# Kernel optimization log

Measured on AMD Instinct MI355X. Metric: run time of the kernel, lower is better.

## Reference

```python
import jax, jax.numpy as jnp
import numpy as np

N, G, P, E = 65536, 256, 256, 1048576   # nodes, graphs, nodes/graph, edges
AF, BF, D, H, L, CE, T = 92, 41, 64, 128, 3, 16, 4
EPS = 1e-5


def _lin(x, W, b):
    return x @ W + b


def setup_inputs() -> dict:
    key = jax.random.key(0)
    ks = jax.random.split(key, 32)
    f = jax.random.normal
    inp = {
        "x": f(ks[0], (N, AF), jnp.float32),
        "edge_attr": f(ks[1], (E, BF), jnp.float32),
        "charge": f(ks[2], (G,), jnp.float32),
        "charge_W": f(ks[3], (1, CE)) * 0.3,
        "charge_b": f(ks[4], (CE,)) * 0.1,
        "atom_W": f(ks[5], (AF + CE, D)) * (1.0 / np.sqrt(AF + CE)),
        "atom_b": f(ks[6], (D,)) * 0.1,
        "bond_W": f(ks[7], (BF, D)) * (1.0 / np.sqrt(BF)),
        "bond_b": f(ks[8], (D,)) * 0.1,
        "nu_W1": f(ks[9], (L, 2 * D, D)) * (1.0 / np.sqrt(2 * D)),
        "nu_b1": f(ks[10], (L, D)) * 0.1,
        "nu_W2": f(ks[11], (L, D, D)) * (1.0 / np.sqrt(D)),
        "nu_b2": f(ks[12], (L, D)) * 0.1,
        "eu_W1": f(ks[13], (L, 3 * D, D)) * (1.0 / np.sqrt(3 * D)),
        "eu_b1": f(ks[14], (L, D)) * 0.1,
        "eu_W2": f(ks[15], (L, D, D)) * (1.0 / np.sqrt(D)),
        "eu_b2": f(ks[16], (L, D)) * 0.1,
        "bn_gamma": jnp.ones((L, D), jnp.float32),
        "bn_beta": jnp.zeros((L, D), jnp.float32),
        "pred_W1": f(ks[17], (D, H)) * (1.0 / np.sqrt(D)),
        "pred_b1": f(ks[18], (H,)) * 0.1,
        "pred_W2": f(ks[19], (H, H)) * (1.0 / np.sqrt(H)),
        "pred_b2": f(ks[20], (H,)) * 0.1,
        "pred_W3": f(ks[21], (H, 1)) * (1.0 / np.sqrt(H)),
        "pred_b3": f(ks[22], (1,)) * 0.1,
        "edge_index": jax.random.randint(ks[23], (2, E), 0, N, jnp.int32),
        "batch": (jnp.arange(N, dtype=jnp.int32) // P),
        "target_site_indices": jax.random.randint(ks[24], (G, T), 0, P, jnp.int32),
    }
    return inp


def reference(x, edge_attr, charge, charge_W, charge_b, atom_W, atom_b, bond_W,
              bond_b, nu_W1, nu_b1, nu_W2, nu_b2, eu_W1, eu_b1, eu_W2, eu_b2,
              bn_gamma, bn_beta, pred_W1, pred_b1, pred_W2, pred_b2, pred_W3,
              pred_b3, edge_index, batch, target_site_indices):
    sp = jax.nn.softplus
    # early charge integration
    charge_feat = _lin(charge[:, None], charge_W, charge_b)        # [G, CE]
    h = _lin(jnp.concatenate([x, charge_feat[batch]], 1), atom_W, atom_b)  # [N, D]
    e = _lin(edge_attr, bond_W, bond_b)                            # [E, D]
    row, col = edge_index[0], edge_index[1]
    for i in range(L):
        hs, hd = h[row], h[col]                                    # gather per edge
        e = _lin(sp(_lin(jnp.concatenate([hs, hd, e], 1), eu_W1[i], eu_b1[i])),
                 eu_W2[i], eu_b2[i])                               # edge update
        m = _lin(sp(_lin(jnp.concatenate([hs, e], 1), nu_W1[i], nu_b1[i])),
                 nu_W2[i], nu_b2[i])                               # messages
        hn = jax.ops.segment_sum(m, col, num_segments=N)           # scatter_add
        mu = hn.mean(0)
        var = hn.var(0)                                            # biased, as torch BN train
        hn = (hn - mu) / jnp.sqrt(var + EPS) * bn_gamma[i] + bn_beta[i]
        h = sp(hn) + h
    # selective pooling over target sites (vectorized version of per-graph loop)
    counts = jax.ops.segment_sum(jnp.ones((N,), h.dtype), batch, num_segments=G)
    counts_i = counts.astype(jnp.int32)
    starts = (jnp.cumsum(counts_i) - counts_i)                     # [G] graph offsets
    valid = target_site_indices < counts_i[:, None]                # [G, T]
    gidx = starts[:, None] + jnp.where(valid, target_site_indices, 0)
    sel = h[gidx] * valid[:, :, None].astype(h.dtype)              # [G, T, D]
    nsel = valid.sum(1)
    sel_mean = sel.sum(1) / jnp.maximum(nsel, 1)[:, None].astype(h.dtype)
    gmean = jax.ops.segment_sum(h, batch, num_segments=G) / counts[:, None]
    graph_repr = jnp.where((nsel > 0)[:, None], sel_mean, gmean)   # [G, D]
    # predictor (dropout = identity in eval)
    z = sp(_lin(graph_repr, pred_W1, pred_b1))
    z = sp(_lin(z, pred_W2, pred_b2))
    out = _lin(z, pred_W3, pred_b3)
    return out.squeeze(-1)                                         # [G]
```

## Files before the change

kernel.cpp:

```cpp
#include <hip/hip_runtime.h>
#include <hip/hip_bf16.h>
#include <hip/hip_fp16.h>
#include <math.h>

#define N_NODES 65536
#define N_GRAPH 256
#define P_NODES 256
#define N_EDGES 1048576
#define AF 92
#define BF 41
#define DIM 64
#define HID 128
#define NLAYER 3
#define CE 16
#define TS 4
#define BN_EPS 1e-5f
#define EPW 32
#define PSTRIDE 33

typedef _Float16 half8 __attribute__((ext_vector_type(8)));
typedef float floatx4 __attribute__((ext_vector_type(4)));

__device__ __forceinline__ float softplus_f(float x) {
    return fmaxf(x, 0.0f) + __logf(1.0f + __expf(-fabsf(x)));
}

__global__ __launch_bounds__(64) void k_h0(
    const float* __restrict__ x, const float* __restrict__ charge,
    const float* __restrict__ chW, const float* __restrict__ chb,
    const float* __restrict__ atomW, const float* __restrict__ atomb,
    const int* __restrict__ batch, float* __restrict__ h)
{
    const int n = blockIdx.x * 64 + threadIdx.x;
    float acc[DIM];
#pragma unroll
    for (int j = 0; j < DIM; ++j) acc[j] = atomb[j];
    const float* xr = x + (size_t)n * AF;
    for (int k2 = 0; k2 < AF; k2 += 2) {
        float2 a = *(const float2*)(xr + k2);
        {
            const float* w = atomW + (size_t)k2 * DIM;
#pragma unroll
            for (int j = 0; j < DIM; ++j) acc[j] = fmaf(w[j], a.x, acc[j]);
        }
        {
            const float* w = atomW + (size_t)(k2 + 1) * DIM;
#pragma unroll
            for (int j = 0; j < DIM; ++j) acc[j] = fmaf(w[j], a.y, acc[j]);
        }
    }
    const float cg = charge[batch[n]];
#pragma unroll
    for (int k = 0; k < CE; ++k) {
        float av = fmaf(cg, chW[k], chb[k]);
        const float* w = atomW + (size_t)(AF + k) * DIM;
#pragma unroll
        for (int j = 0; j < DIM; ++j) acc[j] = fmaf(w[j], av, acc[j]);
    }
    float* hp = h + (size_t)n * DIM;
#pragma unroll
    for (int j = 0; j < DIM; j += 4)
        *(float4*)(hp + j) = make_float4(acc[j], acc[j+1], acc[j+2], acc[j+3]);
}

__global__ __launch_bounds__(256) void k_hist(const int* __restrict__ ecol,
                                              int* __restrict__ cnt)
{
    int t = blockIdx.x * 256 + threadIdx.x;
    atomicAdd(&cnt[ecol[t]], 1);
}

__global__ __launch_bounds__(256) void k_scan(const int* __restrict__ cnt,
                                              int* __restrict__ starts)
{
    __shared__ int ps[256];
    const int t = threadIdx.x;
    int s = 0;
    for (int i = 0; i < 256; ++i) s += cnt[t * 256 + i];
    ps[t] = s;
    __syncthreads();
    for (int off = 1; off < 256; off <<= 1) {
        int v = (t >= off) ? ps[t - off] : 0;
        __syncthreads();
        ps[t] += v;
        __syncthreads();
    }
    int run = ps[t] - s;
    for (int i = 0; i < 256; ++i) {
        starts[t * 256 + i] = run;
        run += cnt[t * 256 + i];
    }
    if (t == 255) starts[N_NODES] = run;
}

__global__ __launch_bounds__(256) void k_scatter(const int* __restrict__ ecol,
                                                 int* __restrict__ cur,
                                                 int* __restrict__ perm,
                                                 int* __restrict__ ipos)
{
    int t = blockIdx.x * 256 + threadIdx.x;
    int pos = atomicAdd(&cur[ecol[t]], 1);
    perm[pos] = t;
    ipos[t] = pos;
}

__global__ __launch_bounds__(256) void k_wprep_all(
    const float* __restrict__ euW1, const float* __restrict__ euW2,
    const float* __restrict__ nuW1, const float* __restrict__ nuW2,
    __half* __restrict__ out)
{
    const int idx = blockIdx.x * 256 + threadIdx.x;
    const int layer = idx / 28672;
    int off = idx - layer * 28672;
    const float* W;
    if (off < 12288)        { W = euW1 + (size_t)layer * 192 * DIM; }
    else if (off < 16384)   { W = euW2 + (size_t)layer * DIM * DIM; off -= 12288; }
    else if (off < 24576)   { W = nuW1 + (size_t)layer * 128 * DIM; off -= 16384; }
    else                    { W = nuW2 + (size_t)layer * DIM * DIM; off -= 24576; }
    int j    = off & 7;
    int lane = (off >> 3) & 63;
    int f    = off >> 9;
    int ntile = f & 3;
    int kIter = f >> 2;
    int k = kIter * 32 + ((lane >> 4) & 3) * 8 + j;
    int n = ntile * 16 + (lane & 15);
    out[idx] = __float2half(W[k * 64 + n]);
}

__global__ __launch_bounds__(256) void k_wprep_bond(
    const float* __restrict__ bondW, __half* __restrict__ out)
{
    const int idx = blockIdx.x * 256 + threadIdx.x;
    int j    = idx & 7;
    int lane = (idx >> 3) & 63;
    int f    = idx >> 9;
    int ntile = f & 3;
    int kIter = f >> 2;
    int k = kIter * 32 + ((lane >> 4) & 3) * 8 + j;
    int n = ntile * 16 + (lane & 15);
    out[idx] = (k < BF) ? __float2half(bondW[k * 64 + n]) : __float2half(0.0f);
}

__device__ __forceinline__ void init_acc(floatx4 acc[2][4],
                                         const float* __restrict__ b, int mrow)
{
#pragma unroll
    for (int n = 0; n < 4; ++n) {
        float bv = b[n * 16 + mrow];
        floatx4 f = {bv, bv, bv, bv};
        acc[0][n] = f;
        acc[1][n] = f;
    }
}

__device__ __forceinline__ void gemm_panel(floatx4 acc[2][4],
                                           const _Float16* __restrict__ P,
                                           const __half* __restrict__ Wf,
                                           int fragBase, int quad,
                                           int mrow, int lane)
{
    const _Float16* Wh = (const _Float16*)Wf;
#pragma unroll
    for (int ki = 0; ki < 2; ++ki) {
        const _Float16* pa = P + (size_t)(((ki * 4 + quad) * PSTRIDE + mrow) * 8);
        half8 a0 = *(const half8*)pa;
        half8 a1 = *(const half8*)(pa + 16 * 8);
#pragma unroll
        for (int n = 0; n < 4; ++n) {
            half8 b = *(const half8*)(Wh +
                ((size_t)(fragBase + ki * 4 + n) * 64 + lane) * 8);
            acc[0][n] = __builtin_amdgcn_mfma_f32_16x16x32_f16(a0, b, acc[0][n], 0, 0, 0);
            acc[1][n] = __builtin_amdgcn_mfma_f32_16x16x32_f16(a1, b, acc[1][n], 0, 0, 0);
        }
    }
}

__device__ __forceinline__ void cstore_panel(const floatx4 acc[2][4],
                                             _Float16* __restrict__ P,
                                             int quad, int mrow, bool sp)
{
#pragma unroll
    for (int t = 0; t < 2; ++t)
#pragma unroll
        for (int n = 0; n < 4; ++n)
#pragma unroll
            for (int r = 0; r < 4; ++r) {
                int edge = t * 16 + quad * 4 + r;
                int d = n * 16 + mrow;
                float v = acc[t][n][r];
                if (sp) v = softplus_f(v);
                P[((d >> 3) * PSTRIDE + edge) * 8 + (d & 7)] = (_Float16)v;
            }
}

__device__ __forceinline__ void rows_to_global(const _Float16* __restrict__ P,
                                               __half* __restrict__ dst,
                                               int e0, int lane)
{
#pragma unroll
    for (int i = 0; i < 4; ++i) {
        int idx = i * 64 + lane;
        int eL = idx >> 3;
        int c  = idx & 7;
        half8 v = *(const half8*)&P[(c * PSTRIDE + eL) * 8];
        *(half8*)((_Float16*)dst + (size_t)(e0 + eL) * 64 + c * 8) = v;
    }
}

__device__ __forceinline__ void stage_h(const float* __restrict__ hrow,
                                        _Float16* __restrict__ P,
                                        int sEdge, int sSeg)
{
    const float* hp = hrow + sSeg * 32;
#pragma unroll
    for (int i = 0; i < 4; ++i) {
        float4 v0 = *(const float4*)(hp + i * 8);
        float4 v1 = *(const float4*)(hp + i * 8 + 4);
        half8 hv;
        hv[0] = (_Float16)v0.x; hv[1] = (_Float16)v0.y;
        hv[2] = (_Float16)v0.z; hv[3] = (_Float16)v0.w;
        hv[4] = (_Float16)v1.x; hv[5] = (_Float16)v1.y;
        hv[6] = (_Float16)v1.z; hv[7] = (_Float16)v1.w;
        *(half8*)&P[((sSeg * 4 + i) * PSTRIDE + sEdge) * 8] = hv;
    }
}

__device__ __forceinline__ void stage_e2(_Float16* __restrict__ P,
                                         int id2, float2 v)
{
    int idx = id2 * 2;
    int e = (idx * 51151) >> 21;
    int k = idx - e * 41;
    P[((k >> 3) * PSTRIDE + e) * 8 + (k & 7)] = (_Float16)v.x;
    idx++;
    e = (idx * 51151) >> 21;
    k = idx - e * 41;
    P[((k >> 3) * PSTRIDE + e) * 8 + (k & 7)] = (_Float16)v.y;
}

__global__ __launch_bounds__(64) void k_e0m(
    const float* __restrict__ eattr, const __half* __restrict__ Wb,
    const float* __restrict__ bondb, const int* __restrict__ ipos,
    __half* __restrict__ eT)
{
    __shared__ __align__(16) _Float16 P0[8 * PSTRIDE * 8];
    __shared__ int slot[32];
    const int lane = threadIdx.x;
    const int quad = lane >> 4;
    const int mrow = lane & 15;
    const int e0   = blockIdx.x * 32;

    if (lane < 32) slot[lane] = ipos[e0 + lane];

    {
        half8 z = {};
#pragma unroll
        for (int i = 0; i < 4; ++i) ((half8*)P0)[i * 64 + lane] = z;
        if (lane < 8) ((half8*)P0)[256 + lane] = z;
    }
    __syncthreads();

    const float* src = eattr + (size_t)e0 * BF;
#pragma unroll
    for (int i = 0; i < 10; ++i) {
        const int id2 = i * 64 + lane;
        float2 v = *(const float2*)(src + id2 * 2);
        stage_e2(P0, id2, v);
    }
    if (lane < 16) {
        const int id2 = 640 + lane;
        float2 v = *(const float2*)(src + id2 * 2);
        stage_e2(P0, id2, v);
    }
    __syncthreads();

    floatx4 acc[2][4];
    init_acc(acc, bondb, mrow);
    gemm_panel(acc, P0, Wb, 0, quad, mrow, lane);
    __syncthreads();
    cstore_panel(acc, P0, quad, mrow, false);
    __syncthreads();

#pragma unroll
    for (int i = 0; i < 4; ++i) {
        int idx = i * 64 + lane;
        int eL = idx >> 3;
        int c  = idx & 7;
        half8 v = *(const half8*)&P0[(c * PSTRIDE + eL) * 8];
        *(half8*)((_Float16*)eT + (size_t)slot[eL] * DIM + c * 8) = v;
    }
}

__global__ __launch_bounds__(64) void k_edge4(
    const float* __restrict__ h, __half* __restrict__ eT,
    const __half* __restrict__ Wf,
    const float* __restrict__ eub1, const float* __restrict__ eub2,
    const float* __restrict__ nub1, const float* __restrict__ nub2,
    const int* __restrict__ erow, const int* __restrict__ ecol,
    const int* __restrict__ perm,
    __half* __restrict__ m)
{
    __shared__ __align__(16) _Float16 P0[8 * PSTRIDE * 8];
    __shared__ __align__(16) _Float16 P1[8 * PSTRIDE * 8];
    const int lane = threadIdx.x;
    const int quad = lane >> 4;
    const int mrow = lane & 15;
    const int e0   = blockIdx.x * EPW;
    const int sEdge = lane >> 1;
    const int sSeg  = lane & 1;

    floatx4 acc[2][4];

    half8 epre[4];
    {
        const _Float16* ep = (const _Float16*)(eT + (size_t)(e0 + sEdge) * DIM) + sSeg * 32;
#pragma unroll
        for (int i = 0; i < 4; ++i) epre[i] = *(const half8*)(ep + i * 8);
    }

    const int ed = perm[e0 + sEdge];
    stage_h(h + (size_t)erow[ed] * DIM, P0, sEdge, sSeg);
    stage_h(h + (size_t)ecol[ed] * DIM, P1, sEdge, sSeg);
    __syncthreads();

    init_acc(acc, eub1, mrow);
    gemm_panel(acc, P0, Wf, 0, quad, mrow, lane);
    gemm_panel(acc, P1, Wf, 8, quad, mrow, lane);
    __syncthreads();
    {
#pragma unroll
        for (int i = 0; i < 4; ++i)
            *(half8*)&P1[((sSeg * 4 + i) * PSTRIDE + sEdge) * 8] = epre[i];
    }
    __syncthreads();
    gemm_panel(acc, P1, Wf, 16, quad, mrow, lane);
    __syncthreads();
    cstore_panel(acc, P1, quad, mrow, true);
    __syncthreads();

    init_acc(acc, eub2, mrow);
    gemm_panel(acc, P1, Wf, 24, quad, mrow, lane);
    __syncthreads();
    cstore_panel(acc, P1, quad, mrow, false);
    __syncthreads();
    rows_to_global(P1, eT, e0, lane);

    init_acc(acc, nub1, mrow);
    gemm_panel(acc, P0, Wf, 32, quad, mrow, lane);
    gemm_panel(acc, P1, Wf, 40, quad, mrow, lane);
    __syncthreads();
    cstore_panel(acc, P0, quad, mrow, true);
    __syncthreads();

    init_acc(acc, nub2, mrow);
    gemm_panel(acc, P0, Wf, 48, quad, mrow, lane);
    __syncthreads();
    cstore_panel(acc, P1, quad, mrow, false);
    __syncthreads();
    rows_to_global(P1, m, e0, lane);
}

__global__ __launch_bounds__(256) void k_agg(
    const __half2* __restrict__ m2, const int* __restrict__ starts,
    float* __restrict__ hn)
{
    const int w = threadIdx.x >> 6;
    const int lane = threadIdx.x & 63;
    const int n = blockIdx.x * 4 + w;
    const int s = starts[n], e = starts[n + 1];
    const int r = lane >> 5, d2 = lane & 31;
    float ax = 0.f, ay = 0.f;
    for (int i = s + r; i < e; i += 2) {
        float2 f = __half22float2(m2[(size_t)i * 32 + d2]);
        ax += f.x; ay += f.y;
    }
    ax += __shfl(ax, lane ^ 32, 64);
    ay += __shfl(ay, lane ^ 32, 64);
    if (r == 0) *(float2*)(hn + (size_t)n * DIM + d2 * 2) = make_float2(ax, ay);
}

__global__ __launch_bounds__(256) void k_bnstats(const float* __restrict__ hn,
                                                 float* __restrict__ stats)
{
    const int j = threadIdx.x & 63;
    const int sub = threadIdx.x >> 6;
    const int r0 = blockIdx.x * 256;
    float s = 0.f, qq = 0.f;
    for (int i = 0; i < 64; ++i) {
        float v = hn[(size_t)(r0 + i * 4 + sub) * DIM + j];
        s += v;
        qq = fmaf(v, v, qq);
    }
    __shared__ float ls[256], lq[256];
    ls[threadIdx.x] = s; lq[threadIdx.x] = qq;
    __syncthreads();
    if (threadIdx.x < 128) {
        ls[threadIdx.x] += ls[threadIdx.x + 128];
        lq[threadIdx.x] += lq[threadIdx.x + 128];
    }
    __syncthreads();
    if (threadIdx.x < 64) {
        atomicAdd(&stats[j],      ls[threadIdx.x] + ls[threadIdx.x + 64]);
        atomicAdd(&stats[64 + j], lq[threadIdx.x] + lq[threadIdx.x + 64]);
    }
}

__global__ __launch_bounds__(256) void k_hupd(
    const float* __restrict__ hn, float* __restrict__ h,
    const float* __restrict__ stats, const float* __restrict__ gamma,
    const float* __restrict__ beta)
{
    const size_t idx = (size_t)blockIdx.x * 256 + threadIdx.x;
    const int j = (int)(idx & 63);
    const float inv_n = 1.0f / (float)N_NODES;
    float mu  = stats[j] * inv_n;
    float var = stats[64 + j] * inv_n - mu * mu;
    float sc  = gamma[j] * rsqrtf(var + BN_EPS);
    float v   = (hn[idx] - mu) * sc + beta[j];
    h[idx] += softplus_f(v);
}

__global__ __launch_bounds__(64) void k_pool(const float* __restrict__ h,
                                             const int* __restrict__ tsi,
                                             float* __restrict__ gr)
{
    const int g = blockIdx.x, j = threadIdx.x;
    float s = 0.f;
#pragma unroll
    for (int t = 0; t < TS; ++t) {
        int p = tsi[g * TS + t];
        s += h[(size_t)(g * P_NODES + p) * DIM + j];
    }
    gr[g * DIM + j] = s * (1.0f / TS);
}

__global__ __launch_bounds__(128) void k_pred(const float* __restrict__ gr,
    const float* __restrict__ W1, const float* __restrict__ b1,
    const float* __restrict__ W2, const float* __restrict__ b2,
    const float* __restrict__ W3, const float* __restrict__ b3,
    float* __restrict__ out)
{
    const int g = blockIdx.x, j = threadIdx.x;
    __shared__ float zin[DIM], z1[HID], red[HID];
    if (j < DIM) zin[j] = gr[g * DIM + j];
    __syncthreads();
    float a = b1[j];
    for (int k = 0; k < DIM; ++k) a = fmaf(zin[k], W1[k * HID + j], a);
    z1[j] = softplus_f(a);
    __syncthreads();
    float a2 = b2[j];
    for (int k = 0; k < HID; ++k) a2 = fmaf(z1[k], W2[k * HID + j], a2);
    red[j] = softplus_f(a2) * W3[j];
    __syncthreads();
    for (int s = 64; s > 0; s >>= 1) {
        if (j < s) red[j] += red[j + s];
        __syncthreads();
    }
    if (j == 0) out[g] = red[0] + b3[0];
}

extern "C" void kernel_launch(void* const* d_in, const int* in_sizes, int n_in,
                              void* d_out, int out_size, void* d_ws, size_t ws_size,
                              hipStream_t stream)
{
    const float* x      = (const float*)d_in[0];
    const float* eattr  = (const float*)d_in[1];
    const float* charge = (const float*)d_in[2];
    const float* chW    = (const float*)d_in[3];
    const float* chb    = (const float*)d_in[4];
    const float* atomW  = (const float*)d_in[5];
    const float* atomb  = (const float*)d_in[6];
    const float* bondW  = (const float*)d_in[7];
    const float* bondb  = (const float*)d_in[8];
    const float* nuW1   = (const float*)d_in[9];
    const float* nub1   = (const float*)d_in[10];
    const float* nuW2   = (const float*)d_in[11];
    const float* nub2   = (const float*)d_in[12];
    const float* euW1   = (const float*)d_in[13];
    const float* eub1   = (const float*)d_in[14];
    const float* euW2   = (const float*)d_in[15];
    const float* eub2   = (const float*)d_in[16];
    const float* gamma  = (const float*)d_in[17];
    const float* beta   = (const float*)d_in[18];
    const float* pW1    = (const float*)d_in[19];
    const float* pb1    = (const float*)d_in[20];
    const float* pW2    = (const float*)d_in[21];
    const float* pb2    = (const float*)d_in[22];
    const float* pW3    = (const float*)d_in[23];
    const float* pb3    = (const float*)d_in[24];
    const int*   eidx   = (const int*)d_in[25];
    const int*   batch  = (const int*)d_in[26];
    const int*   tsi    = (const int*)d_in[27];
    const int* erow = eidx;
    const int* ecol = eidx + N_EDGES;

    char* ws = (char*)d_ws;
    float*  h      = (float*)(ws);
    float*  hn     = (float*)(ws + ((size_t)16 << 20));
    int*    ipos   = (int*)  (ws + ((size_t)16 << 20));
    float*  stats  = (float*)(ws + ((size_t)32 << 20));
    float*  gr     = (float*)(ws + ((size_t)32 << 20) + (64 << 10));
    int*    counts = (int*)  (ws + ((size_t)33 << 20));
    int*    starts = (int*)  (ws + ((size_t)33 << 20) + (256 << 10));
    int*    cur    = (int*)  (ws + ((size_t)33 << 20) + (768 << 10));
    __half* Wfrag  = (__half*)(ws + ((size_t)34 << 20));
    __half* Wbond  = (__half*)(ws + ((size_t)34 << 20) + (256 << 10));
    int*    perm   = (int*)  (ws + ((size_t)35 << 20));
    __half* eT     = (__half*)(ws + ((size_t)40 << 20));
    __half* m      = (__half*)(ws + ((size_t)168 << 20));

    hipMemsetAsync(counts, 0, N_NODES * sizeof(int), stream);
    k_hist<<<N_EDGES / 256, 256, 0, stream>>>(ecol, counts);
    k_scan<<<1, 256, 0, stream>>>(counts, starts);
    hipMemcpyAsync(cur, starts, N_NODES * sizeof(int),
                   hipMemcpyDeviceToDevice, stream);
    k_scatter<<<N_EDGES / 256, 256, 0, stream>>>(ecol, cur, perm, ipos);

    k_wprep_all<<<(3 * 28672) / 256, 256, 0, stream>>>(euW1, euW2, nuW1, nuW2, Wfrag);
    k_wprep_bond<<<16, 256, 0, stream>>>(bondW, Wbond);

    k_h0<<<N_NODES / 64, 64, 0, stream>>>(x, charge, chW, chb, atomW, atomb, batch, h);
    k_e0m<<<N_EDGES / 32, 64, 0, stream>>>(eattr, Wbond, bondb, ipos, eT);

    const size_t LW = 28672;
    for (int i = 0; i < NLAYER; ++i) {
        hipMemsetAsync(stats, 0, 128 * sizeof(float), stream);
        k_edge4<<<N_EDGES / EPW, 64, 0, stream>>>(h, eT, Wfrag + i * LW,
            eub1 + i * DIM, eub2 + i * DIM, nub1 + i * DIM, nub2 + i * DIM,
            erow, ecol, perm, m);
        k_agg<<<N_NODES / 4, 256, 0, stream>>>((const __half2*)m, starts, hn);
        k_bnstats<<<N_NODES / 256, 256, 0, stream>>>(hn, stats);
        k_hupd<<<(N_NODES * DIM) / 256, 256, 0, stream>>>(hn, h, stats,
            gamma + i * DIM, beta + i * DIM);
    }

    k_pool<<<N_GRAPH, 64, 0, stream>>>(h, tsi, gr);
    k_pred<<<N_GRAPH, HID, 0, stream>>>(gr, pW1, pb1, pW2, pb2, pW3, pb3, (float*)d_out);
}
```

Measured before the change: 1.327 ms.

## Fold edge W2 into node W1, keep fp16 node copy, parallelize scan

The edge-update second linear layer and the edge half of the node MLP's first layer are folded into one precomputed 64x64 weight and bias. The node MLP can then run directly from the edge-MLP hidden activations, and the edge output GEMM overlaps with it. A separate fp16 copy of h is maintained so edge kernels gather half-size rows. Messages are stored in the MFMA-native layout and hn becomes fp16, so aggregation and BN passes move less data. The single-block scan is split into a three-kernel parallel scan. Changing the order of operations and using fp16 for hn and the fused weights may alter numerics slightly.

Measured after the change: 1.278 ms. 3.7% less time.

```diff
diff --git a/kernel.cpp b/kernel.cpp
--- a/kernel.cpp
+++ b/kernel.cpp
@@ -19,6 +19,7 @@
 #define PSTRIDE 33
 
 typedef _Float16 half8 __attribute__((ext_vector_type(8)));
+typedef _Float16 half4_t __attribute__((ext_vector_type(4)));
 typedef float floatx4 __attribute__((ext_vector_type(4)));
 
 __device__ __forceinline__ float softplus_f(float x) {
@@ -29,7 +30,8 @@
     const float* __restrict__ x, const float* __restrict__ charge,
     const float* __restrict__ chW, const float* __restrict__ chb,
     const float* __restrict__ atomW, const float* __restrict__ atomb,
-    const int* __restrict__ batch, float* __restrict__ h)
+    const int* __restrict__ batch, float* __restrict__ h,
+    __half* __restrict__ h16)
 {
     const int n = blockIdx.x * 64 + threadIdx.x;
     float acc[DIM];
@@ -58,9 +60,17 @@
         for (int j = 0; j < DIM; ++j) acc[j] = fmaf(w[j], av, acc[j]);
     }
     float* hp = h + (size_t)n * DIM;
+    _Float16* hq = (_Float16*)h16 + (size_t)n * DIM;
 #pragma unroll
     for (int j = 0; j < DIM; j += 4)
         *(float4*)(hp + j) = make_float4(acc[j], acc[j+1], acc[j+2], acc[j+3]);
+#pragma unroll
+    for (int j = 0; j < DIM; j += 8) {
+        half8 hv;
+#pragma unroll
+        for (int u = 0; u < 8; ++u) hv[u] = (_Float16)acc[j + u];
+        *(half8*)(hq + j) = hv;
+    }
 }
 
 __global__ __launch_bounds__(256) void k_hist(const int* __restrict__ ecol,
@@ -70,27 +80,53 @@
     atomicAdd(&cnt[ecol[t]], 1);
 }
 
-__global__ __launch_bounds__(256) void k_scan(const int* __restrict__ cnt,
-                                              int* __restrict__ starts)
+__global__ __launch_bounds__(256) void k_blksum(const int* __restrict__ cnt,
+                                                int* __restrict__ bs)
+{
+    __shared__ int red[256];
+    red[threadIdx.x] = cnt[blockIdx.x * 256 + threadIdx.x];
+    __syncthreads();
+    for (int o = 128; o > 0; o >>= 1) {
+        if (threadIdx.x < o) red[threadIdx.x] += red[threadIdx.x + o];
+        __syncthreads();
+    }
+    if (threadIdx.x == 0) bs[blockIdx.x] = red[0];
+}
+
+__global__ __launch_bounds__(256) void k_scanb(const int* __restrict__ bs,
+                                               int* __restrict__ bo)
 {
     __shared__ int ps[256];
     const int t = threadIdx.x;
-    int s = 0;
-    for (int i = 0; i < 256; ++i) s += cnt[t * 256 + i];
-    ps[t] = s;
+    int v = bs[t];
+    ps[t] = v;
     __syncthreads();
     for (int off = 1; off < 256; off <<= 1) {
-        int v = (t >= off) ? ps[t - off] : 0;
+        int u = (t >= off) ? ps[t - off] : 0;
         __syncthreads();
-        ps[t] += v;
+        ps[t] += u;
         __syncthreads();
     }
-    int run = ps[t] - s;
-    for (int i = 0; i < 256; ++i) {
-        starts[t * 256 + i] = run;
-        run += cnt[t * 256 + i];
-    }
-    if (t == 255) starts[N_NODES] = run;
+    bo[t] = ps[t] - v;
+}
+
+__global__ __launch_bounds__(256) void k_scan3(const int* __restrict__ cnt,
+                                               const int* __restrict__ bo,
+                                               int* __restrict__ starts)
+{
+    __shared__ int ps[256];
+    const int b = blockIdx.x, t = threadIdx.x;
+    int v = cnt[b * 256 + t];
+    ps[t] = v;
+    __syncthreads();
+    for (int off = 1; off < 256; off <<= 1) {
+        int u = (t >= off) ? ps[t - off] : 0;
+        __syncthreads();
+        ps[t] += u;
+        __syncthreads();
+    }
+    starts[b * 256 + t] = bo[b] + ps[t] - v;
+    if (b == 255 && t == 255) starts[N_NODES] = bo[255] + ps[255];
 }
 
 __global__ __launch_bounds__(256) void k_scatter(const int* __restrict__ ecol,
@@ -141,6 +177,45 @@
     out[idx] = (k < BF) ? __float2half(bondW[k * 64 + n]) : __float2half(0.0f);
 }
 
+__global__ __launch_bounds__(64) void k_wfuse(
+    const float* __restrict__ euW2, const float* __restrict__ nuW1,
+    const float* __restrict__ eub2, const float* __restrict__ nub1,
+    float* __restrict__ WfuF32, float* __restrict__ bfu)
+{
+    const int L = blockIdx.x, j = threadIdx.x;
+    const float* W2  = euW2 + (size_t)L * DIM * DIM;
+    const float* N1b = nuW1 + (size_t)L * 128 * DIM + 64 * DIM;
+    float acc[64];
+#pragma unroll
+    for (int k = 0; k < 64; ++k) acc[k] = 0.f;
+    for (int l = 0; l < 64; ++l) {
+        float nv = N1b[l * 64 + j];
+#pragma unroll
+        for (int k = 0; k < 64; ++k) acc[k] = fmaf(W2[k * 64 + l], nv, acc[k]);
+    }
+    float* outW = WfuF32 + (size_t)L * 4096;
+    for (int k = 0; k < 64; ++k) outW[k * 64 + j] = acc[k];
+    float b = nub1[L * 64 + j];
+    for (int l = 0; l < 64; ++l) b = fmaf(eub2[L * 64 + l], N1b[l * 64 + j], b);
+    bfu[L * 64 + j] = b;
+}
+
+__global__ __launch_bounds__(256) void k_wprep_fuse(
+    const float* __restrict__ WfuF32, __half* __restrict__ out)
+{
+    const int idx = blockIdx.x * 256 + threadIdx.x;
+    const int layer = idx >> 12;
+    int off = idx & 4095;
+    int j    = off & 7;
+    int lane = (off >> 3) & 63;
+    int f    = off >> 9;
+    int ntile = f & 3;
+    int kIter = f >> 2;
+    int k = kIter * 32 + ((lane >> 4) & 3) * 8 + j;
+    int n = ntile * 16 + (lane & 15);
+    out[idx] = __float2half(WfuF32[(size_t)layer * 4096 + k * 64 + n]);
+}
+
 __device__ __forceinline__ void init_acc(floatx4 acc[2][4],
                                          const float* __restrict__ b, int mrow)
 {
@@ -207,22 +282,172 @@
     }
 }
 
-__device__ __forceinline__ void stage_h(const float* __restrict__ hrow,
-                                        _Float16* __restrict__ P,
-                                        int sEdge, int sSeg)
-{
-    const float* hp = hrow + sSeg * 32;
+__device__ __forceinline__ void store_m_native(const floatx4 acc[2][4],
+        __half* __restrict__ m, int blk, int quad, int mrow)
+{
+    _Float16* base = (_Float16*)m + (size_t)blk * 2048;
+#pragma unroll
+    for (int t = 0; t < 2; ++t)
+#pragma unroll
+        for (int n = 0; n < 4; ++n) {
+            half4_t hv;
+            hv[0] = (_Float16)acc[t][n][0];
+            hv[1] = (_Float16)acc[t][n][1];
+            hv[2] = (_Float16)acc[t][n][2];
+            hv[3] = (_Float16)acc[t][n][3];
+            *(half4_t*)(base + ((((t * 4 + n) * 4 + quad) * 16 + mrow) * 4)) = hv;
+        }
+}
+
+__device__ __forceinline__ void stage_h16(const __half* __restrict__ hrow,
+                                          _Float16* __restrict__ P,
+                                          int sEdge, int sSeg)
+{
+    const _Float16* hp = (const _Float16*)hrow + sSeg * 32;
 #pragma unroll
     for (int i = 0; i < 4; ++i) {
-        float4 v0 = *(const float4*)(hp + i * 8);
-        float4 v1 = *(const float4*)(hp + i * 8 + 4);
-        half8 hv;
-        hv[0] = (_Float16)v0.x; hv[1] = (_Float16)v0.y;
-        hv[2] = (_Float16)v0.z; hv[3] = (_Float16)v0.w;
-        hv[4] = (_Float16)v1.x; hv[5] = (_Float16)v1.y;
-        hv[6] = (_Float16)v1.z; hv[7] = (_Float16)v1.w;
+        half8 hv = *(const half8*)(hp + i * 8);
         *(half8*)&P[((sSeg * 4 + i) * PSTRIDE + sEdge) * 8] = hv;
     }
+}
+
+__global__ __launch_bounds__(64, 4) void k_edge4(
+    const __half* __restrict__ h16, __half* __restrict__ eT,
+    const __half* __restrict__ Wf, const __half* __restrict__ Wfu,
+    const float* __restrict__ eub1, const float* __restrict__ eub2,
+    const float* __restrict__ bfu,  const float* __restrict__ nub2,
+    const int* __restrict__ erow, const int* __restrict__ ecol,
+    const int* __restrict__ perm,
+    __half* __restrict__ m)
+{
+    __shared__ __align__(16) _Float16 P0[8 * PSTRIDE * 8];
+    __shared__ __align__(16) _Float16 P1[8 * PSTRIDE * 8];
+    const int lane = threadIdx.x;
+    const int quad = lane >> 4;
+    const int mrow = lane & 15;
+    const int e0   = blockIdx.x * EPW;
+    const int sEdge = lane >> 1;
+    const int sSeg  = lane & 1;
+
+    floatx4 acc[2][4], acc2[2][4];
+
+    half8 epre[4];
+    {
+        const _Float16* ep = (const _Float16*)(eT + (size_t)(e0 + sEdge) * DIM) + sSeg * 32;
+#pragma unroll
+        for (int i = 0; i < 4; ++i) epre[i] = *(const half8*)(ep + i * 8);
+    }
+
+    const int ed = perm[e0 + sEdge];
+    stage_h16(h16 + (size_t)erow[ed] * DIM, P0, sEdge, sSeg);
+    stage_h16(h16 + (size_t)ecol[ed] * DIM, P1, sEdge, sSeg);
+    __syncthreads();
+
+    init_acc(acc, eub1, mrow);
+    gemm_panel(acc, P0, Wf, 0, quad, mrow, lane);
+    gemm_panel(acc, P1, Wf, 8, quad, mrow, lane);
+    __syncthreads();
+    {
+#pragma unroll
+        for (int i = 0; i < 4; ++i)
+            *(half8*)&P1[((sSeg * 4 + i) * PSTRIDE + sEdge) * 8] = epre[i];
+    }
+    __syncthreads();
+    gemm_panel(acc, P1, Wf, 16, quad, mrow, lane);
+    __syncthreads();
+    cstore_panel(acc, P1, quad, mrow, true);
+    __syncthreads();
+
+    init_acc(acc, bfu, mrow);
+    gemm_panel(acc, P0, Wf, 32, quad, mrow, lane);
+    gemm_panel(acc, P1, Wfu, 0, quad, mrow, lane);
+    init_acc(acc2, eub2, mrow);
+    gemm_panel(acc2, P1, Wf, 24, quad, mrow, lane);
+    __syncthreads();
+    cstore_panel(acc, P0, quad, mrow, true);
+    __syncthreads();
+
+    init_acc(acc, nub2, mrow);
+    gemm_panel(acc, P0, Wf, 48, quad, mrow, lane);
+    __syncthreads();
+    cstore_panel(acc2, P1, quad, mrow, false);
+    __syncthreads();
+    rows_to_global(P1, eT, e0, lane);
+    store_m_native(acc, m, blockIdx.x, quad, mrow);
+}
+
+__global__ __launch_bounds__(256) void k_agg(
+    const __half* __restrict__ m, const int* __restrict__ starts,
+    __half* __restrict__ hn)
+{
+    const int w = threadIdx.x >> 6;
+    const int lane = threadIdx.x & 63;
+    const int n = blockIdx.x * 4 + w;
+    const int s = starts[n], e = starts[n + 1];
+    const int nn = lane >> 4, mrow = lane & 15;
+    float acc = 0.f;
+    for (int g = s & ~3; g < e; g += 4) {
+        int blk = g >> 5;
+        int off = g & 31;
+        int t = off >> 4, quad = (off >> 2) & 3;
+        half4_t v = *(const half4_t*)((const _Float16*)m + (size_t)blk * 2048
+                     + (((t * 4 + nn) * 4 + quad) * 16 + mrow) * 4);
+        float f0 = (float)v[0], f1 = (float)v[1];
+        float f2 = (float)v[2], f3 = (float)v[3];
+        if (g >= s && g + 3 < e) {
+            acc += (f0 + f1) + (f2 + f3);
+        } else {
+            if (g     >= s && g     < e) acc += f0;
+            if (g + 1 >= s && g + 1 < e) acc += f1;
+            if (g + 2 >= s && g + 2 < e) acc += f2;
+            if (g + 3 >= s && g + 3 < e) acc += f3;
+        }
+    }
+    hn[(size_t)n * DIM + lane] = (__half)acc;
+}
+
+__global__ __launch_bounds__(256) void k_bnstats(const __half* __restrict__ hn,
+                                                 float* __restrict__ stats)
+{
+    const int j = threadIdx.x & 63;
+    const int sub = threadIdx.x >> 6;
+    const int r0 = blockIdx.x * 256;
+    float s = 0.f, qq = 0.f;
+    for (int i = 0; i < 64; ++i) {
+        float v = (float)hn[(size_t)(r0 + i * 4 + sub) * DIM + j];
+        s += v;
+        qq = fmaf(v, v, qq);
+    }
+    __shared__ float ls[256], lq[256];
+    ls[threadIdx.x] = s; lq[threadIdx.x] = qq;
+    __syncthreads();
+    if (threadIdx.x < 128) {
+        ls[threadIdx.x] += ls[threadIdx.x + 128];
+        lq[threadIdx.x] += lq[threadIdx.x + 128];
+    }
+    __syncthreads();
+    if (threadIdx.x < 64) {
+        atomicAdd(&stats[j],      ls[threadIdx.x] + ls[threadIdx.x + 64]);
+        atomicAdd(&stats[64 + j], lq[threadIdx.x] + lq[threadIdx.x + 64]);
+    }
+}
+
+__global__ __launch_bounds__(256) void k_hupd(
+    const __half* __restrict__ hn, float* __restrict__ h,
+    __half* __restrict__ h16,
+    const float* __restrict__ stats, const float* __restrict__ gamma,
+    const float* __restrict__ beta)
+{
+    const size_t idx = (size_t)blockIdx.x * 256 + threadIdx.x;
+    const int j = (int)(idx & 63);
+    const float inv_n = 1.0f / (float)N_NODES;
+    float mu  = stats[j] * inv_n;
+    float var = stats[64 + j] * inv_n - mu * mu;
+    float sc  = gamma[j] * rsqrtf(var + BN_EPS);
+    float v   = ((float)hn[idx] - mu) * sc + beta[j];
+    float nh  = h[idx] + softplus_f(v);
+    h[idx] = nh;
+    h16[idx] = (__half)nh;
 }
 
 __device__ __forceinline__ void stage_e2(_Float16* __restrict__ P,
@@ -289,135 +514,6 @@
         half8 v = *(const half8*)&P0[(c * PSTRIDE + eL) * 8];
         *(half8*)((_Float16*)eT + (size_t)slot[eL] * DIM + c * 8) = v;
     }
-}
-
-__global__ __launch_bounds__(64) void k_edge4(
-    const float* __restrict__ h, __half* __restrict__ eT,
-    const __half* __restrict__ Wf,
-    const float* __restrict__ eub1, const float* __restrict__ eub2,
-    const float* __restrict__ nub1, const float* __restrict__ nub2,
-    const int* __restrict__ erow, const int* __restrict__ ecol,
-    const int* __restrict__ perm,
-    __half* __restrict__ m)
-{
-    __shared__ __align__(16) _Float16 P0[8 * PSTRIDE * 8];
-    __shared__ __align__(16) _Float16 P1[8 * PSTRIDE * 8];
-    const int lane = threadIdx.x;
-    const int quad = lane >> 4;
-    const int mrow = lane & 15;
-    const int e0   = blockIdx.x * EPW;
-    const int sEdge = lane >> 1;
-    const int sSeg  = lane & 1;
-
-    floatx4 acc[2][4];
-
-    half8 epre[4];
-    {
-        const _Float16* ep = (const _Float16*)(eT + (size_t)(e0 + sEdge) * DIM) + sSeg * 32;
-#pragma unroll
-        for (int i = 0; i < 4; ++i) epre[i] = *(const half8*)(ep + i * 8);
-    }
-
-    const int ed = perm[e0 + sEdge];
-    stage_h(h + (size_t)erow[ed] * DIM, P0, sEdge, sSeg);
-    stage_h(h + (size_t)ecol[ed] * DIM, P1, sEdge, sSeg);
-    __syncthreads();
-
-    init_acc(acc, eub1, mrow);
-    gemm_panel(acc, P0, Wf, 0, quad, mrow, lane);
-    gemm_panel(acc, P1, Wf, 8, quad, mrow, lane);
-    __syncthreads();
-    {
-#pragma unroll
-        for (int i = 0; i < 4; ++i)
-            *(half8*)&P1[((sSeg * 4 + i) * PSTRIDE + sEdge) * 8] = epre[i];
-    }
-    __syncthreads();
-    gemm_panel(acc, P1, Wf, 16, quad, mrow, lane);
-    __syncthreads();
-    cstore_panel(acc, P1, quad, mrow, true);
-    __syncthreads();
-
-    init_acc(acc, eub2, mrow);
-    gemm_panel(acc, P1, Wf, 24, quad, mrow, lane);
-    __syncthreads();
-    cstore_panel(acc, P1, quad, mrow, false);
-    __syncthreads();
-    rows_to_global(P1, eT, e0, lane);
-
-    init_acc(acc, nub1, mrow);
-    gemm_panel(acc, P0, Wf, 32, quad, mrow, lane);
-    gemm_panel(acc, P1, Wf, 40, quad, mrow, lane);
-    __syncthreads();
-    cstore_panel(acc, P0, quad, mrow, true);
-    __syncthreads();
-
-    init_acc(acc, nub2, mrow);
-    gemm_panel(acc, P0, Wf, 48, quad, mrow, lane);
-    __syncthreads();
-    cstore_panel(acc, P1, quad, mrow, false);
-    __syncthreads();
-    rows_to_global(P1, m, e0, lane);
-}
-
-__global__ __launch_bounds__(256) void k_agg(
-    const __half2* __restrict__ m2, const int* __restrict__ starts,
-    float* __restrict__ hn)
-{
-    const int w = threadIdx.x >> 6;
-    const int lane = threadIdx.x & 63;
-    const int n = blockIdx.x * 4 + w;
-    const int s = starts[n], e = starts[n + 1];
-    const int r = lane >> 5, d2 = lane & 31;
-    float ax = 0.f, ay = 0.f;
-    for (int i = s + r; i < e; i += 2) {
-        float2 f = __half22float2(m2[(size_t)i * 32 + d2]);
-        ax += f.x; ay += f.y;
-    }
-    ax += __shfl(ax, lane ^ 32, 64);
-    ay += __shfl(ay, lane ^ 32, 64);
-    if (r == 0) *(float2*)(hn + (size_t)n * DIM + d2 * 2) = make_float2(ax, ay);
-}
-
-__global__ __launch_bounds__(256) void k_bnstats(const float* __restrict__ hn,
-                                                 float* __restrict__ stats)
-{
-    const int j = threadIdx.x & 63;
-    const int sub = threadIdx.x >> 6;
-    const int r0 = blockIdx.x * 256;
-    float s = 0.f, qq = 0.f;
-    for (int i = 0; i < 64; ++i) {
-        float v = hn[(size_t)(r0 + i * 4 + sub) * DIM + j];
-        s += v;
-        qq = fmaf(v, v, qq);
-    }
-    __shared__ float ls[256], lq[256];
-    ls[threadIdx.x] = s; lq[threadIdx.x] = qq;
-    __syncthreads();
-    if (threadIdx.x < 128) {
-        ls[threadIdx.x] += ls[threadIdx.x + 128];
-        lq[threadIdx.x] += lq[threadIdx.x + 128];
-    }
-    __syncthreads();
-    if (threadIdx.x < 64) {
-        atomicAdd(&stats[j],      ls[threadIdx.x] + ls[threadIdx.x + 64]);
-        atomicAdd(&stats[64 + j], lq[threadIdx.x] + lq[threadIdx.x + 64]);
-    }
-}
-
-__global__ __launch_bounds__(256) void k_hupd(
-    const float* __restrict__ hn, float* __restrict__ h,
-    const float* __restrict__ stats, const float* __restrict__ gamma,
-    const float* __restrict__ beta)
-{
-    const size_t idx = (size_t)blockIdx.x * 256 + threadIdx.x;
-    const int j = (int)(idx & 63);
-    const float inv_n = 1.0f / (float)N_NODES;
-    float mu  = stats[j] * inv_n;
-    float var = stats[64 + j] * inv_n - mu * mu;
-    float sc  = gamma[j] * rsqrtf(var + BN_EPS);
-    float v   = (hn[idx] - mu) * sc + beta[j];
-    h[idx] += softplus_f(v);
 }
 
 __global__ __launch_bounds__(64) void k_pool(const float* __restrict__ h,
@@ -496,41 +592,53 @@
 
     char* ws = (char*)d_ws;
     float*  h      = (float*)(ws);
-    float*  hn     = (float*)(ws + ((size_t)16 << 20));
+    __half* hn     = (__half*)(ws + ((size_t)16 << 20));
     int*    ipos   = (int*)  (ws + ((size_t)16 << 20));
+    __half* h16    = (__half*)(ws + ((size_t)24 << 20));
     float*  stats  = (float*)(ws + ((size_t)32 << 20));
     float*  gr     = (float*)(ws + ((size_t)32 << 20) + (64 << 10));
+    int*    bs     = (int*)  (ws + ((size_t)32 << 20) + (192 << 10));
+    int*    bo     = (int*)  (ws + ((size_t)32 << 20) + (196 << 10));
     int*    counts = (int*)  (ws + ((size_t)33 << 20));
     int*    starts = (int*)  (ws + ((size_t)33 << 20) + (256 << 10));
     int*    cur    = (int*)  (ws + ((size_t)33 << 20) + (768 << 10));
     __half* Wfrag  = (__half*)(ws + ((size_t)34 << 20));
     __half* Wbond  = (__half*)(ws + ((size_t)34 << 20) + (256 << 10));
+    __half* Wfu    = (__half*)(ws + ((size_t)34 << 20) + (320 << 10));
+    float*  bfu    = (float*)(ws + ((size_t)34 << 20) + (384 << 10));
+    float*  WfuF32 = (float*)(ws + ((size_t)34 << 20) + (448 << 10));
     int*    perm   = (int*)  (ws + ((size_t)35 << 20));
     __half* eT     = (__half*)(ws + ((size_t)40 << 20));
     __half* m      = (__half*)(ws + ((size_t)168 << 20));
 
     hipMemsetAsync(counts, 0, N_NODES * sizeof(int), stream);
     k_hist<<<N_EDGES / 256, 256, 0, stream>>>(ecol, counts);
-    k_scan<<<1, 256, 0, stream>>>(counts, starts);
+    k_blksum<<<256, 256, 0, stream>>>(counts, bs);
+    k_scanb<<<1, 256, 0, stream>>>(bs, bo);
+    k_scan3<<<256, 256, 0, stream>>>(counts, bo, starts);
     hipMemcpyAsync(cur, starts, N_NODES * sizeof(int),
                    hipMemcpyDeviceToDevice, stream);
     k_scatter<<<N_EDGES / 256, 256, 0, stream>>>(ecol, cur, perm, ipos);
 
     k_wprep_all<<<(3 * 28672) / 256, 256, 0, stream>>>(euW1, euW2, nuW1, nuW2, Wfrag);
     k_wprep_bond<<<16, 256, 0, stream>>>(bondW, Wbond);
-
-    k_h0<<<N_NODES / 64, 64, 0, stream>>>(x, charge, chW, chb, atomW, atomb, batch, h);
+    k_wfuse<<<3, 64, 0, stream>>>(euW2, nuW1, eub2, nub1, WfuF32, bfu);
+    k_wprep_fuse<<<48, 256, 0, stream>>>(WfuF32, Wfu);
+
+    k_h0<<<N_NODES / 64, 64, 0, stream>>>(x, charge, chW, chb, atomW, atomb,
+                                          batch, h, h16);
     k_e0m<<<N_EDGES / 32, 64, 0, stream>>>(eattr, Wbond, bondb, ipos, eT);
 
     const size_t LW = 28672;
     for (int i = 0; i < NLAYER; ++i) {
         hipMemsetAsync(stats, 0, 128 * sizeof(float), stream);
-        k_edge4<<<N_EDGES / EPW, 64, 0, stream>>>(h, eT, Wfrag + i * LW,
-            eub1 + i * DIM, eub2 + i * DIM, nub1 + i * DIM, nub2 + i * DIM,
+        k_edge4<<<N_EDGES / EPW, 64, 0, stream>>>(h16, eT, Wfrag + i * LW,
+            Wfu + (size_t)i * 4096,
+            eub1 + i * DIM, eub2 + i * DIM, bfu + i * DIM, nub2 + i * DIM,
             erow, ecol, perm, m);
-        k_agg<<<N_NODES / 4, 256, 0, stream>>>((const __half2*)m, starts, hn);
+        k_agg<<<N_NODES / 4, 256, 0, stream>>>(m, starts, hn);
         k_bnstats<<<N_NODES / 256, 256, 0, stream>>>(hn, stats);
-        k_hupd<<<(N_NODES * DIM) / 256, 256, 0, stream>>>(hn, h, stats,
+        k_hupd<<<(N_NODES * DIM) / 256, 256, 0, stream>>>(hn, h, h16, stats,
             gamma + i * DIM, beta + i * DIM);
     }
 
```
